# Kernel tuning notes

Measured on AMD Instinct MI355X. Metric: run time of the kernel, lower is better.

Reference implementation:

```python
import jax, jax.numpy as jnp
import numpy as np

DIM = 64
HEADS = 4
SHAPE = (2, 64, 64, 64, DIM)  # [n, h, w, d, C] channels-last


def setup_inputs() -> dict:
    key = jax.random.key(0)
    ks = jax.random.split(key, 9)
    s = 1.0 / np.sqrt(DIM)
    return {
        "x": jax.random.normal(ks[0], SHAPE, dtype=jnp.float32),
        "Wk": jax.random.normal(ks[1], (DIM, DIM), dtype=jnp.float32) * s,
        "bk": jax.random.normal(ks[2], (DIM,), dtype=jnp.float32) * 0.01,
        "Wq": jax.random.normal(ks[3], (DIM, DIM), dtype=jnp.float32) * s,
        "bq": jax.random.normal(ks[4], (DIM,), dtype=jnp.float32) * 0.01,
        "Wv": jax.random.normal(ks[5], (DIM, DIM), dtype=jnp.float32) * s,
        "bv": jax.random.normal(ks[6], (DIM,), dtype=jnp.float32) * 0.01,
        "Wr": jax.random.normal(ks[7], (DIM, DIM), dtype=jnp.float32) * s,
        "br": jax.random.normal(ks[8], (DIM,), dtype=jnp.float32) * 0.01,
        "head_count": HEADS,
    }


def reference(x, Wk, bk, Wq, bq, Wv, bv, Wr, br, head_count):
    n, h, w, d, C = x.shape
    N = h * w * d
    H = head_count
    dk = C // H  # head key channels == head value channels (key/value channels = dim)

    xf = x.reshape(n, N, C)  # tokens along flattened spatial axis
    # Conv3d with 1x1x1 kernel == per-token linear projection over channels
    k = xf @ Wk.T + bk  # [n, N, C]
    q = xf @ Wq.T + bq
    v = xf @ Wv.T + bv

    # split channels into contiguous head chunks -> [n, H, dk, N]
    k = k.reshape(n, N, H, dk).transpose(0, 2, 3, 1)
    q = q.reshape(n, N, H, dk).transpose(0, 2, 3, 1)
    v = v.reshape(n, N, H, dk).transpose(0, 2, 3, 1)

    k = jax.nn.softmax(k, axis=3)  # softmax over spatial positions
    q = jax.nn.softmax(q, axis=2)  # softmax over head key channels

    # context = softmax(K) @ V^T : [n, H, dk, dv]
    ctx = jnp.einsum('nhkN,nhvN->nhkv', k, v)
    # attended = context^T @ softmax(Q) : [n, H, dv, N]
    att = jnp.einsum('nhkv,nhkN->nhvN', ctx, q)

    agg = att.transpose(0, 3, 1, 2).reshape(n, N, C)  # concat heads on channels
    out = agg @ Wr.T + br  # reprojection (1x1x1 conv)
    return out.reshape(n, h, w, d, C)
```

## Files before the change

kernel.cpp:

```cpp
#include <hip/hip_runtime.h>
#include <math.h>


#define NTOK 262144
typedef float4 f4;
typedef _Float16 f16;
typedef __attribute__((ext_vector_type(8))) _Float16 f16x8;
typedef __attribute__((ext_vector_type(4))) _Float16 f16x4;
typedef __attribute__((ext_vector_type(4))) float f32x4;

#define WS_S  0
#define WS_Z  2048
#define WS_MH 2176

__device__ __forceinline__ f16x8 cvt8h2(f4 a, f4 b) {
    f16x8 r;
    r[0] = (f16)a.x; r[1] = (f16)a.y; r[2] = (f16)a.z; r[3] = (f16)a.w;
    r[4] = (f16)b.x; r[5] = (f16)b.y; r[6] = (f16)b.z; r[7] = (f16)b.w;
    return r;
}

__global__ __launch_bounds__(256) void k_init(float* __restrict__ ws) {
    int i = blockIdx.x * 256 + threadIdx.x;
    if (i < 2176) ws[i] = 0.0f;
}

__global__ __launch_bounds__(256, 4) void k_ctx(const float* __restrict__ x,
                                                const float* __restrict__ Wk,
                                                const float* __restrict__ Wv,
                                                float* __restrict__ ws) {
    __shared__ float sr[4096];
    __shared__ float zr[256];

    const int tid  = threadIdx.x;
    const int w    = tid >> 6;
    const int lane = tid & 63;
    const int lr   = lane & 15;
    const int ql   = lane >> 4;

    const int nb = blockIdx.x >> 9;
    const int bi = blockIdx.x & 511;
    const long base = (long)nb * NTOK + (long)bi * 512 + (long)w * 128;

    f16x8 wkf[4][2], wvf[4][2];
    #pragma unroll
    for (int h = 0; h < 4; ++h) {
        const float* kr = &Wk[(16 * h + lr) * 64 + 8 * ql];
        const float* vr = &Wv[(16 * h + lr) * 64 + 8 * ql];
        #pragma unroll
        for (int jc = 0; jc < 2; ++jc) {
            wkf[h][jc] = cvt8h2(*(const f4*)&kr[32 * jc], *(const f4*)&kr[32 * jc + 4]);
            wvf[h][jc] = cvt8h2(*(const f4*)&vr[32 * jc], *(const f4*)&vr[32 * jc + 4]);
        }
    }

    const f32x4 zero4 = {0.f, 0.f, 0.f, 0.f};
    f32x4 S[4] = {zero4, zero4, zero4, zero4};
    float z[4] = {0.f, 0.f, 0.f, 0.f};

    f4 L0, L1, L2, L3;
    {
        const float* xp = x + (((size_t)(base + lr)) << 6) + 8 * ql;
        L0 = *(const f4*)xp;        L1 = *(const f4*)(xp + 4);
        L2 = *(const f4*)(xp + 32); L3 = *(const f4*)(xp + 36);
    }

    for (int s = 0; s < 8; ++s) {
        f16x8 a0 = cvt8h2(L0, L1), a1 = cvt8h2(L2, L3);
        if (s < 7) {
            const float* xp = x + (((size_t)(base + (s + 1) * 16 + lr)) << 6) + 8 * ql;
            L0 = *(const f4*)xp;        L1 = *(const f4*)(xp + 4);
            L2 = *(const f4*)(xp + 32); L3 = *(const f4*)(xp + 36);
        }
        #pragma unroll
        for (int h = 0; h < 4; ++h) {
            f32x4 ak = zero4, av = zero4;
            ak = __builtin_amdgcn_mfma_f32_16x16x32_f16(a0, wkf[h][0], ak, 0, 0, 0);
            ak = __builtin_amdgcn_mfma_f32_16x16x32_f16(a1, wkf[h][1], ak, 0, 0, 0);
            av = __builtin_amdgcn_mfma_f32_16x16x32_f16(a0, wvf[h][0], av, 0, 0, 0);
            av = __builtin_amdgcn_mfma_f32_16x16x32_f16(a1, wvf[h][1], av, 0, 0, 0);
            const float e0 = __expf(ak[0]), e1 = __expf(ak[1]);
            const float e2 = __expf(ak[2]), e3 = __expf(ak[3]);
            z[h] += (e0 + e1) + (e2 + e3);
            f16x4 ekf = {(f16)e0, (f16)e1, (f16)e2, (f16)e3};
            f16x4 evf = {(f16)av[0], (f16)av[1], (f16)av[2], (f16)av[3]};
            S[h] = __builtin_amdgcn_mfma_f32_16x16x16f16(ekf, evf, S[h], 0, 0, 0);
        }
    }

    #pragma unroll
    for (int h = 0; h < 4; ++h) {
        z[h] += __shfl_xor(z[h], 16);
        z[h] += __shfl_xor(z[h], 32);
    }

    #pragma unroll
    for (int h = 0; h < 4; ++h) {
        #pragma unroll
        for (int r = 0; r < 4; ++r)
            sr[((w * 4 + h) * 16 + 4 * ql + r) * 16 + lr] = S[h][r];
        if (lane < 16) zr[(w * 4 + h) * 16 + lane] = z[h];
    }
    __syncthreads();
    #pragma unroll
    for (int i = 0; i < 4; ++i) {
        const int idx = i * 256 + tid;
        const float acc = sr[idx] + sr[1024 + idx] + sr[2048 + idx] + sr[3072 + idx];
        atomicAdd(&ws[WS_S + nb * 1024 + idx], acc);
    }
    if (tid < 64) {
        const float acc = zr[tid] + zr[64 + tid] + zr[128 + tid] + zr[192 + tid];
        atomicAdd(&ws[WS_Z + nb * 64 + tid], acc);
    }
}

__global__ __launch_bounds__(256) void k_m(const float* __restrict__ Wr,
                                           const float* __restrict__ bv,
                                           float* __restrict__ ws) {
    const int n = blockIdx.x;
    f16* MH = (f16*)(ws + WS_MH);
    for (int i = threadIdx.x; i < 4096; i += 256) {
        const int c = i >> 6, p = i & 63;
        const int h = p >> 4, kc = p & 15;
        const float rz = 1.0f / ws[WS_Z + n * 64 + p];
        const float* Srow = ws + WS_S + n * 1024 + h * 256 + kc * 16;
        const float* Wrow = Wr + c * 64 + h * 16;
        const float* bvr  = bv + h * 16;
        float acc = 0.f, accb = 0.f;
        #pragma unroll
        for (int vc = 0; vc < 16; ++vc) {
            acc  += Wrow[vc] * Srow[vc];
            accb += Wrow[vc] * bvr[vc];
        }
        MH[n * 4096 + c * 64 + p] = (f16)(acc * rz + accb);
    }
}

__global__ __launch_bounds__(256, 4) void k_out(const float* __restrict__ x,
                                                const float* __restrict__ Wq,
                                                const float* __restrict__ bq,
                                                const float* __restrict__ br,
                                                float* __restrict__ out,
                                                const float* __restrict__ ws) {
    const int tid  = threadIdx.x;
    const int w    = tid >> 6;
    const int lane = tid & 63;
    const int lr   = lane & 15;
    const int ql   = lane >> 4;

    const int nb = blockIdx.x >> 10;
    const int bi = blockIdx.x & 1023;
    const long base = (long)nb * NTOK + (long)bi * 256 + (long)w * 64;

    f16x8 wqf[4][2];
    f16x4 bqh[4];
    #pragma unroll
    for (int h = 0; h < 4; ++h) {
        const float* qr = &Wq[(16 * h + lr) * 64 + 8 * ql];
        #pragma unroll
        for (int jc = 0; jc < 2; ++jc)
            wqf[h][jc] = cvt8h2(*(const f4*)&qr[32 * jc], *(const f4*)&qr[32 * jc + 4]);
        const f4 b = *(const f4*)&bq[16 * h + 4 * ql];
        bqh[h][0] = (f16)b.x; bqh[h][1] = (f16)b.y;
        bqh[h][2] = (f16)b.z; bqh[h][3] = (f16)b.w;
    }
    f16x4 mfa[4][4];
    f16x4 brh[4];
    const f16* MH = (const f16*)(ws + WS_MH) + (size_t)nb * 4096;
    #pragma unroll
    for (int oct = 0; oct < 4; ++oct) {
        #pragma unroll
        for (int pc = 0; pc < 4; ++pc)
            mfa[oct][pc] = *(const f16x4*)&MH[(16 * oct + lr) * 64 + 16 * pc + 4 * ql];
        const f4 b = *(const f4*)&br[16 * oct + 4 * ql];
        brh[oct][0] = (f16)b.x; brh[oct][1] = (f16)b.y;
        brh[oct][2] = (f16)b.z; brh[oct][3] = (f16)b.w;
    }

    const f32x4 zero4 = {0.f, 0.f, 0.f, 0.f};

    f4 L0, L1, L2, L3;
    {
        const float* xp = x + (((size_t)(base + lr)) << 6) + 8 * ql;
        L0 = *(const f4*)xp;        L1 = *(const f4*)(xp + 4);
        L2 = *(const f4*)(xp + 32); L3 = *(const f4*)(xp + 36);
    }

    for (int s = 0; s < 4; ++s) {
        f16x8 b0 = cvt8h2(L0, L1), b1 = cvt8h2(L2, L3);
        if (s < 3) {
            const float* xp = x + (((size_t)(base + (s + 1) * 16 + lr)) << 6) + 8 * ql;
            L0 = *(const f4*)xp;        L1 = *(const f4*)(xp + 4);
            L2 = *(const f4*)(xp + 32); L3 = *(const f4*)(xp + 36);
        }
        f16x4 qf[4];
        #pragma unroll
        for (int h = 0; h < 4; ++h) {
            f32x4 aq = zero4;
            aq = __builtin_amdgcn_mfma_f32_16x16x32_f16(wqf[h][0], b0, aq, 0, 0, 0);
            aq = __builtin_amdgcn_mfma_f32_16x16x32_f16(wqf[h][1], b1, aq, 0, 0, 0);
            float q0 = aq[0] + (float)bqh[h][0], q1 = aq[1] + (float)bqh[h][1];
            float q2 = aq[2] + (float)bqh[h][2], q3 = aq[3] + (float)bqh[h][3];
            float mx = fmaxf(fmaxf(q0, q1), fmaxf(q2, q3));
            mx = fmaxf(mx, __shfl_xor(mx, 16));
            mx = fmaxf(mx, __shfl_xor(mx, 32));
            float e0 = __expf(q0 - mx), e1 = __expf(q1 - mx);
            float e2 = __expf(q2 - mx), e3 = __expf(q3 - mx);
            float sm = (e0 + e1) + (e2 + e3);
            sm += __shfl_xor(sm, 16);
            sm += __shfl_xor(sm, 32);
            const float rs = 1.0f / sm;
            qf[h][0] = (f16)(e0 * rs); qf[h][1] = (f16)(e1 * rs);
            qf[h][2] = (f16)(e2 * rs); qf[h][3] = (f16)(e3 * rs);
        }
        const size_t obase = ((size_t)(base + s * 16 + lr)) << 6;
        #pragma unroll
        for (int oct = 0; oct < 4; ++oct) {
            f32x4 o = zero4;
            #pragma unroll
            for (int pc = 0; pc < 4; ++pc)
                o = __builtin_amdgcn_mfma_f32_16x16x16f16(mfa[oct][pc], qf[pc], o, 0, 0, 0);
            const f4 res = {o[0] + (float)brh[oct][0], o[1] + (float)brh[oct][1],
                            o[2] + (float)brh[oct][2], o[3] + (float)brh[oct][3]};
            *(f4*)&out[obase + 16 * oct + 4 * ql] = res;
        }
    }
}

extern "C" void kernel_launch(void* const* d_in, const int* in_sizes, int n_in,
                              void* d_out, int out_size, void* d_ws, size_t ws_size,
                              hipStream_t stream) {
    const float* x  = (const float*)d_in[0];
    const float* Wk = (const float*)d_in[1];
    const float* Wq = (const float*)d_in[3];
    const float* bq = (const float*)d_in[4];
    const float* Wv = (const float*)d_in[5];
    const float* bv = (const float*)d_in[6];
    const float* Wr = (const float*)d_in[7];
    const float* br = (const float*)d_in[8];
    float* out = (float*)d_out;
    float* ws  = (float*)d_ws;

    hipLaunchKernelGGL(k_init, dim3(9),    dim3(256), 0, stream, ws);
    hipLaunchKernelGGL(k_ctx,  dim3(1024), dim3(256), 0, stream, x, Wk, Wv, ws);
    hipLaunchKernelGGL(k_m,    dim3(2),    dim3(256), 0, stream, Wr, bv, ws);
    hipLaunchKernelGGL(k_out,  dim3(2048), dim3(256), 0, stream, x, Wq, bq, br, out, ws);
}
```

Measured before the change: 125.4 us.

## Split heads across wave pairs in ctx kernel, widen k_m grid, nontemporal output stores

In k_ctx each wave now handles two of the four heads over twice as many tokens, with a two-deep load pipeline using separate A/B register sets. This halves the per-wave weight registers and the shared-memory reduction. k_m is spread over 32 blocks instead of 2 to cut its serial latency. k_out loads the bias values directly in fp32 inside the loop instead of keeping fp16 register copies, and writes output with nontemporal stores, which also fixes the bias precision loss.

```diff
diff --git a/kernel.cpp b/kernel.cpp
--- a/kernel.cpp
+++ b/kernel.cpp
@@ -29,111 +29,144 @@
                                                 const float* __restrict__ Wk,
                                                 const float* __restrict__ Wv,
                                                 float* __restrict__ ws) {
-    __shared__ float sr[4096];
-    __shared__ float zr[256];
+    __shared__ float sr[2048];
+    __shared__ float zr[128];
 
     const int tid  = threadIdx.x;
     const int w    = tid >> 6;
     const int lane = tid & 63;
     const int lr   = lane & 15;
     const int ql   = lane >> 4;
+    const int hp   = w & 1;
+    const int tw   = w >> 1;
 
     const int nb = blockIdx.x >> 9;
     const int bi = blockIdx.x & 511;
-    const long base = (long)nb * NTOK + (long)bi * 512 + (long)w * 128;
-
-    f16x8 wkf[4][2], wvf[4][2];
-    #pragma unroll
-    for (int h = 0; h < 4; ++h) {
-        const float* kr = &Wk[(16 * h + lr) * 64 + 8 * ql];
-        const float* vr = &Wv[(16 * h + lr) * 64 + 8 * ql];
+    const long base = (long)nb * NTOK + (long)bi * 512 + (long)tw * 256;
+
+    f16x8 wkf[2][2], wvf[2][2];
+    #pragma unroll
+    for (int lh = 0; lh < 2; ++lh) {
+        const int g = 2 * hp + lh;
+        const float* kr = &Wk[(16 * g + lr) * 64 + 8 * ql];
+        const float* vr = &Wv[(16 * g + lr) * 64 + 8 * ql];
         #pragma unroll
         for (int jc = 0; jc < 2; ++jc) {
-            wkf[h][jc] = cvt8h2(*(const f4*)&kr[32 * jc], *(const f4*)&kr[32 * jc + 4]);
-            wvf[h][jc] = cvt8h2(*(const f4*)&vr[32 * jc], *(const f4*)&vr[32 * jc + 4]);
+            wkf[lh][jc] = cvt8h2(*(const f4*)&kr[32 * jc], *(const f4*)&kr[32 * jc + 4]);
+            wvf[lh][jc] = cvt8h2(*(const f4*)&vr[32 * jc], *(const f4*)&vr[32 * jc + 4]);
         }
     }
 
     const f32x4 zero4 = {0.f, 0.f, 0.f, 0.f};
-    f32x4 S[4] = {zero4, zero4, zero4, zero4};
-    float z[4] = {0.f, 0.f, 0.f, 0.f};
-
-    f4 L0, L1, L2, L3;
+    f32x4 S[2] = {zero4, zero4};
+    float z[2] = {0.f, 0.f};
+
+    f4 A0, A1, A2, A3, B0, B1, B2, B3;
     {
         const float* xp = x + (((size_t)(base + lr)) << 6) + 8 * ql;
-        L0 = *(const f4*)xp;        L1 = *(const f4*)(xp + 4);
-        L2 = *(const f4*)(xp + 32); L3 = *(const f4*)(xp + 36);
-    }
-
-    for (int s = 0; s < 8; ++s) {
-        f16x8 a0 = cvt8h2(L0, L1), a1 = cvt8h2(L2, L3);
-        if (s < 7) {
-            const float* xp = x + (((size_t)(base + (s + 1) * 16 + lr)) << 6) + 8 * ql;
-            L0 = *(const f4*)xp;        L1 = *(const f4*)(xp + 4);
-            L2 = *(const f4*)(xp + 32); L3 = *(const f4*)(xp + 36);
-        }
-        #pragma unroll
-        for (int h = 0; h < 4; ++h) {
-            f32x4 ak = zero4, av = zero4;
-            ak = __builtin_amdgcn_mfma_f32_16x16x32_f16(a0, wkf[h][0], ak, 0, 0, 0);
-            ak = __builtin_amdgcn_mfma_f32_16x16x32_f16(a1, wkf[h][1], ak, 0, 0, 0);
-            av = __builtin_amdgcn_mfma_f32_16x16x32_f16(a0, wvf[h][0], av, 0, 0, 0);
-            av = __builtin_amdgcn_mfma_f32_16x16x32_f16(a1, wvf[h][1], av, 0, 0, 0);
-            const float e0 = __expf(ak[0]), e1 = __expf(ak[1]);
-            const float e2 = __expf(ak[2]), e3 = __expf(ak[3]);
-            z[h] += (e0 + e1) + (e2 + e3);
-            f16x4 ekf = {(f16)e0, (f16)e1, (f16)e2, (f16)e3};
-            f16x4 evf = {(f16)av[0], (f16)av[1], (f16)av[2], (f16)av[3]};
-            S[h] = __builtin_amdgcn_mfma_f32_16x16x16f16(ekf, evf, S[h], 0, 0, 0);
-        }
-    }
-
+        A0 = *(const f4*)xp;        A1 = *(const f4*)(xp + 4);
+        A2 = *(const f4*)(xp + 32); A3 = *(const f4*)(xp + 36);
+        const float* yp = x + (((size_t)(base + 16 + lr)) << 6) + 8 * ql;
+        B0 = *(const f4*)yp;        B1 = *(const f4*)(yp + 4);
+        B2 = *(const f4*)(yp + 32); B3 = *(const f4*)(yp + 36);
+    }
+
+    #pragma unroll 2
+    for (int ss = 0; ss < 8; ++ss) {
+        const int s = 2 * ss;
+        {
+            f16x8 a0 = cvt8h2(A0, A1), a1 = cvt8h2(A2, A3);
+            if (s + 2 < 16) {
+                const float* xp = x + (((size_t)(base + (s + 2) * 16 + lr)) << 6) + 8 * ql;
+                A0 = *(const f4*)xp;        A1 = *(const f4*)(xp + 4);
+                A2 = *(const f4*)(xp + 32); A3 = *(const f4*)(xp + 36);
+            }
+            #pragma unroll
+            for (int lh = 0; lh < 2; ++lh) {
+                f32x4 ak = zero4, av = zero4;
+                ak = __builtin_amdgcn_mfma_f32_16x16x32_f16(a0, wkf[lh][0], ak, 0, 0, 0);
+                ak = __builtin_amdgcn_mfma_f32_16x16x32_f16(a1, wkf[lh][1], ak, 0, 0, 0);
+                av = __builtin_amdgcn_mfma_f32_16x16x32_f16(a0, wvf[lh][0], av, 0, 0, 0);
+                av = __builtin_amdgcn_mfma_f32_16x16x32_f16(a1, wvf[lh][1], av, 0, 0, 0);
+                const float e0 = __expf(ak[0]), e1 = __expf(ak[1]);
+                const float e2 = __expf(ak[2]), e3 = __expf(ak[3]);
+                z[lh] += (e0 + e1) + (e2 + e3);
+                f16x4 ekf = {(f16)e0, (f16)e1, (f16)e2, (f16)e3};
+                f16x4 evf = {(f16)av[0], (f16)av[1], (f16)av[2], (f16)av[3]};
+                S[lh] = __builtin_amdgcn_mfma_f32_16x16x16f16(ekf, evf, S[lh], 0, 0, 0);
+            }
+        }
+        {
+            f16x8 a0 = cvt8h2(B0, B1), a1 = cvt8h2(B2, B3);
+            if (s + 3 < 16) {
+                const float* xp = x + (((size_t)(base + (s + 3) * 16 + lr)) << 6) + 8 * ql;
+                B0 = *(const f4*)xp;        B1 = *(const f4*)(xp + 4);
+                B2 = *(const f4*)(xp + 32); B3 = *(const f4*)(xp + 36);
+            }
+            #pragma unroll
+            for (int lh = 0; lh < 2; ++lh) {
+                f32x4 ak = zero4, av = zero4;
+                ak = __builtin_amdgcn_mfma_f32_16x16x32_f16(a0, wkf[lh][0], ak, 0, 0, 0);
+                ak = __builtin_amdgcn_mfma_f32_16x16x32_f16(a1, wkf[lh][1], ak, 0, 0, 0);
+                av = __builtin_amdgcn_mfma_f32_16x16x32_f16(a0, wvf[lh][0], av, 0, 0, 0);
+                av = __builtin_amdgcn_mfma_f32_16x16x32_f16(a1, wvf[lh][1], av, 0, 0, 0);
+                const float e0 = __expf(ak[0]), e1 = __expf(ak[1]);
+                const float e2 = __expf(ak[2]), e3 = __expf(ak[3]);
+                z[lh] += (e0 + e1) + (e2 + e3);
+                f16x4 ekf = {(f16)e0, (f16)e1, (f16)e2, (f16)e3};
+                f16x4 evf = {(f16)av[0], (f16)av[1], (f16)av[2], (f16)av[3]};
+                S[lh] = __builtin_amdgcn_mfma_f32_16x16x16f16(ekf, evf, S[lh], 0, 0, 0);
+            }
+        }
+    }
+
+    #pragma unroll
+    for (int lh = 0; lh < 2; ++lh) {
+        z[lh] += __shfl_xor(z[lh], 16);
+        z[lh] += __shfl_xor(z[lh], 32);
+    }
+
+    #pragma unroll
+    for (int lh = 0; lh < 2; ++lh) {
+        #pragma unroll
+        for (int r = 0; r < 4; ++r)
+            sr[(w * 2 + lh) * 256 + (4 * ql + r) * 16 + lr] = S[lh][r];
+        if (lane < 16) zr[(w * 2 + lh) * 16 + lane] = z[lh];
+    }
+    __syncthreads();
     #pragma unroll
     for (int h = 0; h < 4; ++h) {
-        z[h] += __shfl_xor(z[h], 16);
-        z[h] += __shfl_xor(z[h], 32);
-    }
-
-    #pragma unroll
-    for (int h = 0; h < 4; ++h) {
-        #pragma unroll
-        for (int r = 0; r < 4; ++r)
-            sr[((w * 4 + h) * 16 + 4 * ql + r) * 16 + lr] = S[h][r];
-        if (lane < 16) zr[(w * 4 + h) * 16 + lane] = z[h];
-    }
-    __syncthreads();
-    #pragma unroll
-    for (int i = 0; i < 4; ++i) {
-        const int idx = i * 256 + tid;
-        const float acc = sr[idx] + sr[1024 + idx] + sr[2048 + idx] + sr[3072 + idx];
-        atomicAdd(&ws[WS_S + nb * 1024 + idx], acc);
+        const int hp2 = h >> 1, lh = h & 1;
+        const float a2 = sr[(hp2 * 2 + lh) * 256 + tid] + sr[((hp2 + 2) * 2 + lh) * 256 + tid];
+        atomicAdd(&ws[WS_S + nb * 1024 + h * 256 + tid], a2);
     }
     if (tid < 64) {
-        const float acc = zr[tid] + zr[64 + tid] + zr[128 + tid] + zr[192 + tid];
-        atomicAdd(&ws[WS_Z + nb * 64 + tid], acc);
+        const int h = tid >> 4, kc = tid & 15;
+        const int hp2 = h >> 1, lh = h & 1;
+        const float a2 = zr[(hp2 * 2 + lh) * 16 + kc] + zr[((hp2 + 2) * 2 + lh) * 16 + kc];
+        atomicAdd(&ws[WS_Z + nb * 64 + tid], a2);
     }
 }
 
 __global__ __launch_bounds__(256) void k_m(const float* __restrict__ Wr,
                                            const float* __restrict__ bv,
                                            float* __restrict__ ws) {
-    const int n = blockIdx.x;
+    const int n = blockIdx.x >> 4;
+    const int i = (blockIdx.x & 15) * 256 + threadIdx.x;
     f16* MH = (f16*)(ws + WS_MH);
-    for (int i = threadIdx.x; i < 4096; i += 256) {
-        const int c = i >> 6, p = i & 63;
-        const int h = p >> 4, kc = p & 15;
-        const float rz = 1.0f / ws[WS_Z + n * 64 + p];
-        const float* Srow = ws + WS_S + n * 1024 + h * 256 + kc * 16;
-        const float* Wrow = Wr + c * 64 + h * 16;
-        const float* bvr  = bv + h * 16;
-        float acc = 0.f, accb = 0.f;
-        #pragma unroll
-        for (int vc = 0; vc < 16; ++vc) {
-            acc  += Wrow[vc] * Srow[vc];
-            accb += Wrow[vc] * bvr[vc];
-        }
-        MH[n * 4096 + c * 64 + p] = (f16)(acc * rz + accb);
-    }
+    const int c = i >> 6, p = i & 63;
+    const int h = p >> 4, kc = p & 15;
+    const float rz = 1.0f / ws[WS_Z + n * 64 + p];
+    const float* Srow = ws + WS_S + n * 1024 + h * 256 + kc * 16;
+    const float* Wrow = Wr + c * 64 + h * 16;
+    const float* bvr  = bv + h * 16;
+    float acc = 0.f, accb = 0.f;
+    #pragma unroll
+    for (int vc = 0; vc < 16; ++vc) {
+        acc  += Wrow[vc] * Srow[vc];
+        accb += Wrow[vc] * bvr[vc];
+    }
+    MH[n * 4096 + c * 64 + p] = (f16)(acc * rz + accb);
 }
 
 __global__ __launch_bounds__(256, 4) void k_out(const float* __restrict__ x,
@@ -153,29 +186,20 @@
     const long base = (long)nb * NTOK + (long)bi * 256 + (long)w * 64;
 
     f16x8 wqf[4][2];
-    f16x4 bqh[4];
     #pragma unroll
     for (int h = 0; h < 4; ++h) {
         const float* qr = &Wq[(16 * h + lr) * 64 + 8 * ql];
         #pragma unroll
         for (int jc = 0; jc < 2; ++jc)
             wqf[h][jc] = cvt8h2(*(const f4*)&qr[32 * jc], *(const f4*)&qr[32 * jc + 4]);
-        const f4 b = *(const f4*)&bq[16 * h + 4 * ql];
-        bqh[h][0] = (f16)b.x; bqh[h][1] = (f16)b.y;
-        bqh[h][2] = (f16)b.z; bqh[h][3] = (f16)b.w;
     }
     f16x4 mfa[4][4];
-    f16x4 brh[4];
     const f16* MH = (const f16*)(ws + WS_MH) + (size_t)nb * 4096;
     #pragma unroll
-    for (int oct = 0; oct < 4; ++oct) {
+    for (int oct = 0; oct < 4; ++oct)
         #pragma unroll
         for (int pc = 0; pc < 4; ++pc)
             mfa[oct][pc] = *(const f16x4*)&MH[(16 * oct + lr) * 64 + 16 * pc + 4 * ql];
-        const f4 b = *(const f4*)&br[16 * oct + 4 * ql];
-        brh[oct][0] = (f16)b.x; brh[oct][1] = (f16)b.y;
-        brh[oct][2] = (f16)b.z; brh[oct][3] = (f16)b.w;
-    }
 
     const f32x4 zero4 = {0.f, 0.f, 0.f, 0.f};
 
@@ -199,8 +223,9 @@
             f32x4 aq = zero4;
             aq = __builtin_amdgcn_mfma_f32_16x16x32_f16(wqf[h][0], b0, aq, 0, 0, 0);
             aq = __builtin_amdgcn_mfma_f32_16x16x32_f16(wqf[h][1], b1, aq, 0, 0, 0);
-            float q0 = aq[0] + (float)bqh[h][0], q1 = aq[1] + (float)bqh[h][1];
-            float q2 = aq[2] + (float)bqh[h][2], q3 = aq[3] + (float)bqh[h][3];
+            const f4 bqv = *(const f4*)&bq[16 * h + 4 * ql];
+            float q0 = aq[0] + bqv.x, q1 = aq[1] + bqv.y;
+            float q2 = aq[2] + bqv.z, q3 = aq[3] + bqv.w;
             float mx = fmaxf(fmaxf(q0, q1), fmaxf(q2, q3));
             mx = fmaxf(mx, __shfl_xor(mx, 16));
             mx = fmaxf(mx, __shfl_xor(mx, 32));
@@ -220,9 +245,11 @@
             #pragma unroll
             for (int pc = 0; pc < 4; ++pc)
                 o = __builtin_amdgcn_mfma_f32_16x16x16f16(mfa[oct][pc], qf[pc], o, 0, 0, 0);
-            const f4 res = {o[0] + (float)brh[oct][0], o[1] + (float)brh[oct][1],
-                            o[2] + (float)brh[oct][2], o[3] + (float)brh[oct][3]};
-            *(f4*)&out[obase + 16 * oct + 4 * ql] = res;
+            const f4 brv = *(const f4*)&br[16 * oct + 4 * ql];
+            f32x4 res;
+            res[0] = o[0] + brv.x; res[1] = o[1] + brv.y;
+            res[2] = o[2] + brv.z; res[3] = o[3] + brv.w;
+            __builtin_nontemporal_store(res, (f32x4*)&out[obase + 16 * oct + 4 * ql]);
         }
     }
 }
@@ -243,6 +270,6 @@
 
     hipLaunchKernelGGL(k_init, dim3(9),    dim3(256), 0, stream, ws);
     hipLaunchKernelGGL(k_ctx,  dim3(1024), dim3(256), 0, stream, x, Wk, Wv, ws);
-    hipLaunchKernelGGL(k_m,    dim3(2),    dim3(256), 0, stream, Wr, bv, ws);
+    hipLaunchKernelGGL(k_m,    dim3(32),   dim3(256), 0, stream, Wr, bv, ws);
     hipLaunchKernelGGL(k_out,  dim3(2048), dim3(256), 0, stream, x, Wq, bq, br, out, ws);
 }
```

New measurement: 152.6 us. 1.22x slower.
